# Performance work log

Hardware: AMD Instinct MI355X
Metric: run time of the kernel (lower is better)

Reference implementation:

```python
import jax, jax.numpy as jnp
import numpy as np

B, T, NV, DEG, E = 64, 256, 20000, 8, 128
NSEG, NBUCKET = NV * DEG, 288
F_DIST, F_DIR, F_TT, HID = 50, 50, 50, 100
FEED = 2 * E + F_DIST + F_DIR  # 356


def setup_inputs() -> dict:
    key = jax.random.key(0)
    ks = jax.random.split(key, 32)
    s = 1.0 / np.sqrt(E)
    return {
        "xs_padded": jax.random.randint(ks[0], (B, T), 0, NV),
        "lengths": jax.random.randint(ks[1], (B,), 8, T + 1),
        "xs_actions": jax.random.randint(ks[2], (B, T - 1), 0, DEG),
        "destinations": jax.random.randint(ks[3], (B,), 0, NV),
        "adj_list": jax.random.randint(ks[4], (NV, DEG), 0, NV),
        "seg_ids": jax.random.randint(ks[5], (NV, DEG), 0, NSEG),
        "start_time": 42,
        "locations": jax.random.normal(ks[6], (NV, 2)),
        "time_dist_seg": jax.random.uniform(ks[7], (NSEG, NBUCKET)) * 10.0,
        "emb": jax.random.normal(ks[8], (NV + 2, E)) * 0.01,
        "Wq": jax.random.normal(ks[9], (E, E)) * s,
        "Wk": jax.random.normal(ks[10], (E, E)) * s,
        "Wv": jax.random.normal(ks[11], (E, E)) * s,
        "Wo": jax.random.normal(ks[12], (E, E)) * s,
        "dist_W": jax.random.normal(ks[13], (1, F_DIST)),
        "dist_b": jnp.zeros((F_DIST,)),
        "dir_W": jax.random.normal(ks[14], (2, F_DIR)) * 0.7,
        "dir_b": jnp.zeros((F_DIR,)),
        "tt_W": jax.random.normal(ks[15], (1, F_TT)),
        "tt_b": jnp.zeros((F_TT,)),
        "ob_W1": jax.random.normal(ks[16], (F_TT, F_TT // 2)) * (1.0 / np.sqrt(F_TT)),
        "ob_b1": jnp.zeros((F_TT // 2,)),
        "ob_W2": jax.random.normal(ks[17], (F_TT // 2, 1)) * (1.0 / np.sqrt(F_TT // 2)),
        "ob_b2": jnp.zeros((1,)),
        "om_W1": jax.random.normal(ks[18], (FEED, HID)) * (1.0 / np.sqrt(FEED)),
        "om_b1": jnp.zeros((HID,)),
        "om_W2": jax.random.normal(ks[19], (HID, HID // 2)) * (1.0 / np.sqrt(HID)),
        "om_b2": jnp.zeros((HID // 2,)),
        "om_W3": jax.random.normal(ks[20], (HID // 2, 1)) * (1.0 / np.sqrt(HID // 2)),
        "om_b3": jnp.zeros((1,)),
    }


def reference(xs_padded, lengths, xs_actions, destinations, adj_list, seg_ids,
              start_time, locations, time_dist_seg, emb, Wq, Wk, Wv, Wo,
              dist_W, dist_b, dir_W, dir_b, tt_W, tt_b,
              ob_W1, ob_b1, ob_W2, ob_b2,
              om_W1, om_b1, om_W2, om_b2, om_W3, om_b3):
    # --- embeddings + causal/padding-masked self-attention (flash_att) ---
    x_e = emb[xs_padded]                                       # [B,T,E]
    q, k, v = x_e @ Wq, x_e @ Wk, x_e @ Wv
    scores = jnp.einsum('bqe,bke->bqk', q, k) / jnp.sqrt(jnp.float32(E))
    causal = jnp.triu(jnp.ones((T, T), bool), 1)
    pad = jnp.arange(T)[None, :] >= lengths[:, None]           # key padding [B,T]
    scores = jnp.where(causal[None] | pad[:, None, :], -1e9, scores)
    hidden = jnp.einsum('bqk,bke->bqe', jax.nn.softmax(scores, axis=-1), v) @ Wo

    # --- irregular neighbor gather: route_neighbors only filled for t < len-1 ---
    valid_t = jnp.arange(T)[None, :] < (lengths - 1)[:, None]  # [B,T]
    rn = jnp.where(valid_t[:, :, None], adj_list[xs_padded], 0)  # [B,T,DEG]

    # --- distance to destination feature ---
    dest_c = locations[destinations][:, None, None, :]         # [B,1,1,2]
    nbr_c = locations[rn]                                      # [B,T,DEG,2]
    dist = jnp.abs(nbr_c - dest_c).sum(-1, keepdims=True) * 100.0
    dist_f = dist @ dist_W + dist_b

    # --- direction (unit vector) feature ---
    vec = nbr_c - locations[xs_padded][:, :, None, :]
    unit = vec / (jnp.linalg.norm(vec, axis=-1, keepdims=True) + 1e-8)
    dir_f = unit @ dir_W + dir_b

    # --- travel-time lookup + masked whitening ---
    nmask = rn != 0
    tt = time_dist_seg[seg_ids[xs_padded], start_time]         # [B,T,DEG]
    mf = nmask.astype(tt.dtype)
    cnt = mf.sum()
    mean = (tt * mf).sum() / cnt
    var = (((tt - mean) ** 2) * mf).sum() / (cnt - 1.0)        # unbiased, like torch.std
    tt = (tt - mean) / (jnp.sqrt(var) + 1e-6)
    tt_f = (tt[..., None] @ tt_W + tt_b) * mf[..., None]

    # --- fuse and score neighbors ---
    hid_e = jnp.broadcast_to(hidden[:, :, None, :], (B, T, DEG, E))
    dest_e = jnp.broadcast_to(emb[destinations][:, None, None, :], (B, T, DEG, E))
    feed = jnp.concatenate([hid_e, dist_f, dir_f, dest_e], axis=-1)  # [B,T,DEG,356]

    ob = (jax.nn.relu(tt_f @ ob_W1 + ob_b1) @ ob_W2 + ob_b2).squeeze(-1)
    h1 = jax.nn.relu(feed @ om_W1 + om_b1)
    h2 = jax.nn.relu(h1 @ om_W2 + om_b2)
    logits = (h2 @ om_W3 + om_b3).squeeze(-1) + ob             # [B,T,DEG]

    # --- per-route mean cross-entropy over valid transitions, summed over batch ---
    logp = jax.nn.log_softmax(logits[:, :T - 1], axis=-1)
    nll = -jnp.take_along_axis(logp, xs_actions[..., None], axis=-1).squeeze(-1)
    vmask = (jnp.arange(T - 1)[None, :] < (lengths - 1)[:, None]).astype(nll.dtype)
    per = (nll * vmask).sum(1) / (lengths - 1).astype(nll.dtype)
    return per.sum()
```

## Files before the change

### kernel.cpp

```cpp
#include <hip/hip_runtime.h>
#include <math.h>

#define BB 64
#define TT 256
#define DEG 8
#define EE 128
#define NBUCKET 288
#define HID 100
#define H2 50

constexpr size_t OFF_STATS   = 0;
constexpr size_t OFF_CDIST   = 4;
constexpr size_t OFF_CDIRX   = 104;
constexpr size_t OFF_CDIRY   = 204;
constexpr size_t OFF_BASE    = 304;
constexpr size_t OFF_V25     = 404;
constexpr size_t OFF_C25     = 429;
constexpr size_t OFF_OBZ     = 454;
constexpr size_t OFF_DESTPRE = 456;
constexpr size_t OFF_WF      = 6856;
constexpr size_t OFF_TT      = 32456;
constexpr size_t OFF_Q       = 163528;
constexpr size_t OFF_K       = OFF_Q + 16384 * 128;
constexpr size_t OFF_VP      = OFF_K + 16384 * 128;

__global__ void __launch_bounds__(256) k_setup(
    const int* destinations, const float* emb, const float* Wo,
    const float* dist_W, const float* dist_b, const float* dir_W, const float* dir_b,
    const float* tt_W, const float* tt_b, const float* ob_W1, const float* ob_b1,
    const float* ob_W2, const float* ob_b2, const float* om_W1, const float* om_b1,
    float* ws, float* out) {
    __shared__ float sh[EE];
    int blk = blockIdx.x;
    int j = threadIdx.x;
    if (blk == 0) {
        if (j < 4) ws[OFF_STATS + j] = 0.f;
        if (j == 0) out[0] = 0.f;
        if (j < HID) {
            float cd = 0.f, cx = 0.f, cy = 0.f, bs = om_b1[j];
            for (int f = 0; f < 50; f++) {
                float w1d = om_W1[(128 + f) * HID + j];
                float w1r = om_W1[(178 + f) * HID + j];
                cd += dist_W[f] * w1d;
                bs += dist_b[f] * w1d + dir_b[f] * w1r;
                cx += dir_W[f] * w1r;
                cy += dir_W[50 + f] * w1r;
            }
            ws[OFF_CDIST + j] = cd; ws[OFF_CDIRX + j] = cx;
            ws[OFF_CDIRY + j] = cy; ws[OFF_BASE + j] = bs;
        }
        if (j >= 128 && j < 153) {
            int jj = j - 128;
            float v = 0.f, c = ob_b1[jj];
            for (int i = 0; i < 50; i++) {
                v += tt_W[i] * ob_W1[i * 25 + jj];
                c += tt_b[i] * ob_W1[i * 25 + jj];
            }
            ws[OFF_V25 + jj] = v; ws[OFF_C25 + jj] = c;
        }
        if (j == 200) {
            float z = ob_b2[0];
            for (int i = 0; i < 25; i++) z += fmaxf(ob_b1[i], 0.f) * ob_W2[i];
            ws[OFF_OBZ] = z;
        }
    } else if (blk <= 64) {
        int b = blk - 1;
        if (j < EE) sh[j] = emb[(size_t)destinations[b] * EE + j];
        __syncthreads();
        if (j < HID) {
            float acc = 0.f;
            for (int i = 0; i < EE; i++) acc += sh[i] * om_W1[(228 + i) * HID + j];
            ws[OFF_DESTPRE + b * HID + j] = acc;
        }
    } else {
        int i = blk - 65;
        if (j < EE) sh[j] = Wo[i * EE + j];
        __syncthreads();
        if (j < HID) {
            float acc = 0.f;
            for (int jj = 0; jj < EE; jj++) acc += sh[jj] * om_W1[jj * HID + j];
            ws[OFF_WF + i * HID + j] = acc;
        }
    }
}

__global__ void __launch_bounds__(256) k_mid(
    const int* xs, const int* lengths, const int* adj, const int* seg,
    const int* stime, const float* tds, const float* emb,
    const float* Wq, const float* Wk, const float* Wv, float* ws) {
    __shared__ float smem[2 * 128 * 36 + 32];
    int blk = blockIdx.x;
    int tid = threadIdx.x;
    if (blk < 512) {
        float (*XT)[36]  = (float(*)[36])smem;
        float (*T1T)[36] = (float(*)[36])(smem + 128 * 36);
        int* vids = (int*)(smem + 2 * 128 * 36);
        int r0 = blk * 32;
        if (tid < 32) vids[tid] = xs[r0 + tid];
        __syncthreads();
        for (int c = 0; c < 16; c++) {
            int idx = c * 256 + tid;
            int r = idx >> 7, i = idx & 127;
            XT[i][r] = emb[(size_t)vids[r] * EE + i];
        }
        __syncthreads();
        int cg = tid & 31, rg = tid >> 5;
        const float* Wmats[2] = {Wq, Wk};
        float* Omats[2] = {ws + OFF_Q, ws + OFF_K};
        for (int mtx = 0; mtx < 2; mtx++) {
            const float* W = Wmats[mtx];
            float acc[4][4];
            #pragma unroll
            for (int a = 0; a < 4; a++)
                #pragma unroll
                for (int bb = 0; bb < 4; bb++) acc[a][bb] = 0.f;
            #pragma unroll 4
            for (int i = 0; i < EE; i++) {
                float4 av = *(const float4*)&XT[i][rg << 2];
                float4 wv = *(const float4*)&W[i * EE + (cg << 2)];
                acc[0][0] += av.x * wv.x; acc[0][1] += av.x * wv.y; acc[0][2] += av.x * wv.z; acc[0][3] += av.x * wv.w;
                acc[1][0] += av.y * wv.x; acc[1][1] += av.y * wv.y; acc[1][2] += av.y * wv.z; acc[1][3] += av.y * wv.w;
                acc[2][0] += av.z * wv.x; acc[2][1] += av.z * wv.y; acc[2][2] += av.z * wv.z; acc[2][3] += av.z * wv.w;
                acc[3][0] += av.w * wv.x; acc[3][1] += av.w * wv.y; acc[3][2] += av.w * wv.z; acc[3][3] += av.w * wv.w;
            }
            float* O = Omats[mtx];
            #pragma unroll
            for (int jj = 0; jj < 4; jj++)
                *(float4*)&O[(size_t)(r0 + (rg << 2) + jj) * EE + (cg << 2)] =
                    make_float4(acc[jj][0], acc[jj][1], acc[jj][2], acc[jj][3]);
        }
        {
            float acc[4][4];
            #pragma unroll
            for (int a = 0; a < 4; a++)
                #pragma unroll
                for (int bb = 0; bb < 4; bb++) acc[a][bb] = 0.f;
            #pragma unroll 4
            for (int i = 0; i < EE; i++) {
                float4 av = *(const float4*)&XT[i][rg << 2];
                float4 wv = *(const float4*)&Wv[i * EE + (cg << 2)];
                acc[0][0] += av.x * wv.x; acc[0][1] += av.x * wv.y; acc[0][2] += av.x * wv.z; acc[0][3] += av.x * wv.w;
                acc[1][0] += av.y * wv.x; acc[1][1] += av.y * wv.y; acc[1][2] += av.y * wv.z; acc[1][3] += av.y * wv.w;
                acc[2][0] += av.z * wv.x; acc[2][1] += av.z * wv.y; acc[2][2] += av.z * wv.z; acc[2][3] += av.z * wv.w;
                acc[3][0] += av.w * wv.x; acc[3][1] += av.w * wv.y; acc[3][2] += av.w * wv.z; acc[3][3] += av.w * wv.w;
            }
            #pragma unroll
            for (int jj = 0; jj < 4; jj++)
                #pragma unroll
                for (int ii = 0; ii < 4; ii++)
                    T1T[(cg << 2) + ii][(rg << 2) + jj] = acc[jj][ii];
        }
        __syncthreads();
        if (cg < 25) {
            const float* WF = ws + OFF_WF;
            float acc[4][4];
            #pragma unroll
            for (int a = 0; a < 4; a++)
                #pragma unroll
                for (int bb = 0; bb < 4; bb++) acc[a][bb] = 0.f;
            #pragma unroll 4
            for (int i = 0; i < EE; i++) {
                float4 av = *(const float4*)&T1T[i][rg << 2];
                float4 wv = *(const float4*)&WF[i * HID + (cg << 2)];
                acc[0][0] += av.x * wv.x; acc[0][1] += av.x * wv.y; acc[0][2] += av.x * wv.z; acc[0][3] += av.x * wv.w;
                acc[1][0] += av.y * wv.x; acc[1][1] += av.y * wv.y; acc[1][2] += av.y * wv.z; acc[1][3] += av.y * wv.w;
                acc[2][0] += av.z * wv.x; acc[2][1] += av.z * wv.y; acc[2][2] += av.z * wv.z; acc[2][3] += av.z * wv.w;
                acc[3][0] += av.w * wv.x; acc[3][1] += av.w * wv.y; acc[3][2] += av.w * wv.z; acc[3][3] += av.w * wv.w;
            }
            float* VP = ws + OFF_VP;
            #pragma unroll
            for (int jj = 0; jj < 4; jj++)
                *(float4*)&VP[(size_t)(r0 + (rg << 2) + jj) * HID + (cg << 2)] =
                    make_float4(acc[jj][0], acc[jj][1], acc[jj][2], acc[jj][3]);
        }
    } else {
        float* rs = smem; float* rq = smem + 256; float* rc = smem + 512;
        int st = *stime;
        float lsum = 0.f, lsq = 0.f, lcnt = 0.f;
        int total = BB * TT * DEG;
        for (int idx = (blk - 512) * 256 + tid; idx < total; idx += 256 * 256) {
            int d = idx & 7;
            int bt = idx >> 3;
            int t = bt & 255;
            int b = bt >> 8;
            int len = lengths[b];
            if (t >= len - 1) continue;
            int v = xs[bt];
            int sg = seg[v * DEG + d];
            float tt = tds[(size_t)sg * NBUCKET + st];
            ws[OFF_TT + idx] = tt;
            int a = adj[v * DEG + d];
            if (a != 0) { lsum += tt; lsq += tt * tt; lcnt += 1.f; }
        }
        rs[tid] = lsum; rq[tid] = lsq; rc[tid] = lcnt;
        __syncthreads();
        for (int s = 128; s > 0; s >>= 1) {
            if (tid < s) { rs[tid] += rs[tid + s]; rq[tid] += rq[tid + s]; rc[tid] += rc[tid + s]; }
            __syncthreads();
        }
        if (tid == 0) {
            atomicAdd(&ws[OFF_STATS + 0], rs[0]);
            atomicAdd(&ws[OFF_STATS + 1], rq[0]);
            atomicAdd(&ws[OFF_STATS + 2], rc[0]);
        }
    }
}

__global__ void __launch_bounds__(256) k_attnfinal(
    const int* lengths, const int* xs, const int* xs_actions,
    const int* destinations, const int* adj, const float* locations,
    const float* om_W2, const float* om_b2, const float* om_W3, const float* om_b3,
    const float* ob_W2, const float* ob_b2,
    float* ws, float* out) {
    int blk = blockIdx.x;
    int tile = 31 - (blk >> 6);
    int b = blk & 63;
    int t0 = tile << 3;
    int len = lengths[b];
    if (t0 >= len - 1) return;
    int nqv = len - 1 - t0; if (nqv > 8) nqv = 8;
    int nk = t0 + 8;
    __shared__ float smem[13160];
    float (*H1P)[104] = (float(*)[104])smem;
    float (*Qs)[132]  = (float(*)[132])(smem + 832);
    float (*S)[260]   = (float(*)[260])(smem + 1888);
    float (*Vs)[104]  = (float(*)[104])(smem + 3968);
    float (*pacc)[8]  = (float(*)[8])(smem + 10624);
    float (*W2s)[56]  = (float(*)[56])(smem + 832);
    float (*h1T)[64]  = (float(*)[64])(smem + 6432);
    float* distR = smem + 12832;
    float* uxR   = smem + 12896;
    float* uyR   = smem + 12960;
    float* obR   = smem + 13024;
    float* lgS   = smem + 13088;
    float* nllS  = smem + 13152;
    int tid = threadIdx.x;
    if (tid < 8) nllS[tid] = 0.f;
    {
        const float* Qg = ws + OFF_Q + (size_t)(b * TT + t0) * EE;
        int r = tid >> 5, c4 = (tid & 31) << 2;
        *(float4*)&Qs[r][c4] = *(const float4*)&Qg[r * EE + c4];
    }
    __syncthreads();
    {
        const float* Kg = ws + OFF_K + (size_t)(b * TT) * EE;
        int w = tid >> 6;
        int key = (tid >> 2) & 15, chunk = tid & 3;
        int coff = chunk << 5;
        for (int k0 = w << 4; k0 < nk; k0 += 64) {
            int kk = k0 + key;
            if (kk < nk) {
                float4 kf[8];
                const float4* Kr = (const float4*)&Kg[(size_t)kk * EE + coff];
                #pragma unroll
                for (int j = 0; j < 8; j++) kf[j] = Kr[j];
                #pragma unroll
                for (int q = 0; q < 8; q++) {
                    const float4* qr = (const float4*)&Qs[q][coff];
                    float s = 0.f;
                    #pragma unroll
                    for (int j = 0; j < 8; j++) {
                        float4 a = qr[j], x = kf[j];
                        s += a.x * x.x + a.y * x.y + a.z * x.z + a.w * x.w;
                    }
                    s += __shfl_xor(s, 1, 64);
                    s += __shfl_xor(s, 2, 64);
                    if (chunk == 0) S[q][kk] = s * 0.08838834764831845f;
                }
            }
        }
    }
    __syncthreads();
    if (tid < 128) {
        int q = tid >> 4, li = tid & 15;
        int tq = t0 + q;
        float sreg[16];
        float mx = -1e30f;
        #pragma unroll
        for (int m = 0; m < 16; m++) {
            int k = li + (m << 4);
            float sv = (k < nk && k <= tq) ? S[q][k] : -1e30f;
            sreg[m] = sv;
            mx = fmaxf(mx, sv);
        }
        #pragma unroll
        for (int o = 1; o < 16; o <<= 1) mx = fmaxf(mx, __shfl_xor(mx, o, 16));
        float ls = 0.f;
        #pragma unroll
        for (int m = 0; m < 16; m++) {
            float p = __expf(sreg[m] - mx);
            sreg[m] = p; ls += p;
        }
        #pragma unroll
        for (int o = 1; o < 16; o <<= 1) ls += __shfl_xor(ls, o, 16);
        float inv = 1.f / ls;
        #pragma unroll
        for (int m = 0; m < 16; m++) S[q][li + (m << 4)] = sreg[m] * inv;
    }
    __syncthreads();
    {
        int kc = tid >> 7;
        int q = (tid >> 4) & 7, cg = tid & 15;
        float acc[8];
        #pragma unroll
        for (int j = 0; j < 8; j++) acc[j] = 0.f;
        const float* VPg = ws + OFF_VP + (size_t)(b * TT) * HID;
        for (int vt0 = 0; vt0 < nk; vt0 += 64) {
            __syncthreads();
            int nrow = nk - vt0; if (nrow > 64) nrow = 64;
            for (int idx = tid; idx < nrow * 25; idx += 256) {
                int r = idx / 25, c4 = (idx - r * 25) << 2;
                *(float4*)&Vs[r][c4] = *(const float4*)&VPg[(size_t)(vt0 + r) * HID + c4];
            }
            __syncthreads();
            int base = vt0 + (kc << 5);
            int kmax = nk - base; if (kmax > 32) kmax = 32;
            if (cg < 13) {
                for (int k = 0; k < kmax; k++) {
                    float p = S[q][base + k];
                    const float4* vr = (const float4*)&Vs[(kc << 5) + k][cg << 3];
                    float4 v0 = vr[0], v1 = vr[1];
                    acc[0] += p * v0.x; acc[1] += p * v0.y;
                    acc[2] += p * v0.z; acc[3] += p * v0.w;
                    acc[4] += p * v1.x; acc[5] += p * v1.y;
                    acc[6] += p * v1.z; acc[7] += p * v1.w;
                }
            }
        }
        if (kc == 1 && cg < 13) {
            float* pp = pacc[(q << 4) + cg];
            #pragma unroll
            for (int j = 0; j < 8; j++) pp[j] = acc[j];
        }
        __syncthreads();
        if (kc == 0 && cg < 13) {
            const float* pp = pacc[(q << 4) + cg];
            const float* BASEv = ws + OFF_BASE;
            const float* DP = ws + OFF_DESTPRE + b * HID;
            int c0 = cg << 3;
            #pragma unroll
            for (int j = 0; j < 8; j++) {
                int c = c0 + j;
                if (c < HID) H1P[q][c] = acc[j] + pp[j] + BASEv[c] + DP[c];
            }
        }
    }
    __syncthreads();
    for (int idx = tid; idx < 5600; idx += 256) {
        int mm = idx / 56, n = idx - mm * 56;
        W2s[mm][n] = (n < H2) ? om_W2[mm * H2 + n] : 0.f;
    }
    float smean, sdinv;
    {
        float sum = ws[OFF_STATS], sq = ws[OFF_STATS + 1], cnt = ws[OFF_STATS + 2];
        smean = sum / cnt;
        float var = (sq - cnt * smean * smean) / (cnt - 1.f);
        sdinv = 1.f / (sqrtf(var) + 1e-6f);
    }
    if (tid < 64) {
        int ql = tid >> 3, d = tid & 7;
        int t = t0 + ql;
        int bt = b * TT + t;
        int v = xs[bt];
        int a = adj[v * DEG + d];
        float nbx = locations[2 * a], nby = locations[2 * a + 1];
        int dst = destinations[b];
        float dxl = locations[2 * dst], dyl = locations[2 * dst + 1];
        float cxl = locations[2 * v], cyl = locations[2 * v + 1];
        distR[tid] = (fabsf(nbx - dxl) + fabsf(nby - dyl)) * 100.f;
        float vx = nbx - cxl, vy = nby - cyl;
        float nrm = sqrtf(vx * vx + vy * vy) + 1e-8f;
        uxR[tid] = vx / nrm; uyR[tid] = vy / nrm;
        float ttn = (ws[OFF_TT + (size_t)bt * 8 + d] - smean) * sdinv;
        float obp = 0.f;
        for (int j = 0; j < 25; j++)
            obp += fmaxf(ttn * ws[OFF_V25 + j] + ws[OFF_C25 + j], 0.f) * ob_W2[j];
        obR[tid] = (a != 0) ? (obp + ob_b2[0]) : ws[OFF_OBZ];
    }
    __syncthreads();
    {
        int r = tid & 63, mq = tid >> 6;
        int qa = r >> 3;
        float dv = distR[r], ux = uxR[r], uy = uyR[r];
        const float* CD = ws + OFF_CDIST;
        const float* CX = ws + OFF_CDIRX;
        const float* CY = ws + OFF_CDIRY;
        const float* Hq = H1P[qa];
        int m0 = mq * 25;
        #pragma unroll 5
        for (int mi = 0; mi < 25; mi++) {
            int m = m0 + mi;
            float pre = Hq[m] + dv * CD[m] + ux * CX[m] + uy * CY[m];
            h1T[m][r] = fmaxf(pre, 0.f);
        }
    }
    __syncthreads();
    {
        int lane = tid & 63, w = tid >> 6;
        int rg = (w << 2) | (lane >> 4);
        int half = (lane >> 3) & 1;
        int cg = lane & 7;
        int r0 = rg << 2, n0 = cg << 3;
        float facc[4][8];
        #pragma unroll
        for (int jr = 0; jr < 4; jr++)
            #pragma unroll
            for (int k = 0; k < 8; k++) facc[jr][k] = 0.f;
        if (cg < 7) {
            int m0 = half * 50;
            #pragma unroll 5
            for (int mi = 0; mi < 50; mi++) {
                int m = m0 + mi;
                float4 hv = *(const float4*)&h1T[m][r0];
                float4 w0 = *(const float4*)&W2s[m][n0];
                float4 w1 = *(const float4*)&W2s[m][n0 + 4];
                facc[0][0] += hv.x * w0.x; facc[0][1] += hv.x * w0.y; facc[0][2] += hv.x * w0.z; facc[0][3] += hv.x * w0.w;
                facc[0][4] += hv.x * w1.x; facc[0][5] += hv.x * w1.y; facc[0][6] += hv.x * w1.z; facc[0][7] += hv.x * w1.w;
                facc[1][0] += hv.y * w0.x; facc[1][1] += hv.y * w0.y; facc[1][2] += hv.y * w0.z; facc[1][3] += hv.y * w0.w;
                facc[1][4] += hv.y * w1.x; facc[1][5] += hv.y * w1.y; facc[1][6] += hv.y * w1.z; facc[1][7] += hv.y * w1.w;
                facc[2][0] += hv.z * w0.x; facc[2][1] += hv.z * w0.y; facc[2][2] += hv.z * w0.z; facc[2][3] += hv.z * w0.w;
                facc[2][4] += hv.z * w1.x; facc[2][5] += hv.z * w1.y; facc[2][6] += hv.z * w1.z; facc[2][7] += hv.z * w1.w;
                facc[3][0] += hv.w * w0.x; facc[3][1] += hv.w * w0.y; facc[3][2] += hv.w * w0.z; facc[3][3] += hv.w * w0.w;
                facc[3][4] += hv.w * w1.x; facc[3][5] += hv.w * w1.y; facc[3][6] += hv.w * w1.z; facc[3][7] += hv.w * w1.w;
            }
        }
        #pragma unroll
        for (int jr = 0; jr < 4; jr++)
            #pragma unroll
            for (int k = 0; k < 8; k++)
                facc[jr][k] += __shfl_xor(facc[jr][k], 8, 64);
        float parts[4] = {0.f, 0.f, 0.f, 0.f};
        if (cg < 7) {
            float b2v[8], w3v[8];
            #pragma unroll
            for (int k = 0; k < 8; k++) {
                int n = n0 + k;
                b2v[k] = (n < H2) ? om_b2[n] : 0.f;
                w3v[k] = (n < H2) ? om_W3[n] : 0.f;
            }
            #pragma unroll
            for (int jr = 0; jr < 4; jr++) {
                float part = 0.f;
                #pragma unroll
                for (int k = 0; k < 8; k++)
                    part += fmaxf(facc[jr][k] + b2v[k], 0.f) * w3v[k];
                parts[jr] = part;
            }
        }
        float ob3 = om_b3[0];
        #pragma unroll
        for (int jr = 0; jr < 4; jr++) {
            float part = parts[jr];
            part += __shfl_xor(part, 1, 64);
            part += __shfl_xor(part, 2, 64);
            part += __shfl_xor(part, 4, 64);
            if ((lane & 15) == 0) lgS[r0 + jr] = part + ob3 + obR[r0 + jr];
        }
    }
    __syncthreads();
    if (tid < 8) {
        int qa = tid;
        if (qa < nqv) {
            float lg[8];
            float mxl = -1e30f;
            #pragma unroll
            for (int d = 0; d < 8; d++) {
                lg[d] = lgS[(qa << 3) + d];
                mxl = fmaxf(mxl, lg[d]);
            }
            int act = xs_actions[b * (TT - 1) + t0 + qa];
            float se = 0.f, sel = 0.f;
            #pragma unroll
            for (int d = 0; d < 8; d++) {
                se += __expf(lg[d] - mxl);
                if (d == act) sel = lg[d];
            }
            float nll = mxl + __logf(se) - sel;
            nllS[qa] = nll / (float)(len - 1);
        }
    }
    __syncthreads();
    if (tid == 0) {
        float s = 0.f;
        #pragma unroll
        for (int i = 0; i < 8; i++) s += nllS[i];
        atomicAdd(out, s);
    }
}

extern "C" void kernel_launch(void* const* d_in, const int* in_sizes, int n_in,
                              void* d_out, int out_size, void* d_ws, size_t ws_size,
                              hipStream_t stream) {
    const int* xs_padded    = (const int*)d_in[0];
    const int* lengths      = (const int*)d_in[1];
    const int* xs_actions   = (const int*)d_in[2];
    const int* destinations = (const int*)d_in[3];
    const int* adj_list     = (const int*)d_in[4];
    const int* seg_ids      = (const int*)d_in[5];
    const int* start_time   = (const int*)d_in[6];
    const float* locations  = (const float*)d_in[7];
    const float* tds        = (const float*)d_in[8];
    const float* emb        = (const float*)d_in[9];
    const float* Wq         = (const float*)d_in[10];
    const float* Wk         = (const float*)d_in[11];
    const float* Wv         = (const float*)d_in[12];
    const float* Wo         = (const float*)d_in[13];
    const float* dist_W     = (const float*)d_in[14];
    const float* dist_b     = (const float*)d_in[15];
    const float* dir_W      = (const float*)d_in[16];
    const float* dir_b      = (const float*)d_in[17];
    const float* tt_W       = (const float*)d_in[18];
    const float* tt_b       = (const float*)d_in[19];
    const float* ob_W1      = (const float*)d_in[20];
    const float* ob_b1      = (const float*)d_in[21];
    const float* ob_W2      = (const float*)d_in[22];
    const float* ob_b2      = (const float*)d_in[23];
    const float* om_W1      = (const float*)d_in[24];
    const float* om_b1      = (const float*)d_in[25];
    const float* om_W2      = (const float*)d_in[26];
    const float* om_b2      = (const float*)d_in[27];
    const float* om_W3      = (const float*)d_in[28];
    const float* om_b3      = (const float*)d_in[29];
    float* ws  = (float*)d_ws;
    float* out = (float*)d_out;

    k_setup<<<193, 256, 0, stream>>>(destinations, emb, Wo, dist_W, dist_b,
                                     dir_W, dir_b, tt_W, tt_b, ob_W1, ob_b1,
                                     ob_W2, ob_b2, om_W1, om_b1, ws, out);
    k_mid<<<768, 256, 0, stream>>>(xs_padded, lengths, adj_list, seg_ids,
                                   start_time, tds, emb, Wq, Wk, Wv, ws);
    k_attnfinal<<<BB * 32, 256, 0, stream>>>(
        lengths, xs_padded, xs_actions, destinations, adj_list, locations,
        om_W2, om_b2, om_W3, om_b3, ob_W2, ob_b2, ws, out);
}
```

Baseline: 442.5 us.

## Shrink attention-final shared memory to raise occupancy and stream weights from global

Cuts the k_attnfinal shared footprint from about 52KB to about 21KB. It drops the V staging tile, the padded W2 copy and the h1T buffer. P·V now reads value rows straight from global memory, and om_W2 is pre-padded to 56 columns once in k_setup and read from global/cache inside the MLP loop. The first-layer ReLU activations are recomputed inline from H1P plus per-neighbor coefficients instead of being stored. The feature computation moves onto otherwise idle threads during softmax, and launch bounds ask for 6 blocks per CU. The trade is more global/L2 traffic and recomputation in exchange for higher occupancy and fewer barriers.

```diff
diff --git a/kernel.cpp b/kernel.cpp
--- a/kernel.cpp
+++ b/kernel.cpp
@@ -19,6 +19,7 @@
 constexpr size_t OFF_OBZ     = 454;
 constexpr size_t OFF_DESTPRE = 456;
 constexpr size_t OFF_WF      = 6856;
+constexpr size_t OFF_W2P     = 19656;
 constexpr size_t OFF_TT      = 32456;
 constexpr size_t OFF_Q       = 163528;
 constexpr size_t OFF_K       = OFF_Q + 16384 * 128;
@@ -29,7 +30,7 @@
     const float* dist_W, const float* dist_b, const float* dir_W, const float* dir_b,
     const float* tt_W, const float* tt_b, const float* ob_W1, const float* ob_b1,
     const float* ob_W2, const float* ob_b2, const float* om_W1, const float* om_b1,
-    float* ws, float* out) {
+    const float* om_W2, float* ws, float* out) {
     __shared__ float sh[EE];
     int blk = blockIdx.x;
     int j = threadIdx.x;
@@ -72,7 +73,7 @@
             for (int i = 0; i < EE; i++) acc += sh[i] * om_W1[(228 + i) * HID + j];
             ws[OFF_DESTPRE + b * HID + j] = acc;
         }
-    } else {
+    } else if (blk <= 192) {
         int i = blk - 65;
         if (j < EE) sh[j] = Wo[i * EE + j];
         __syncthreads();
@@ -80,6 +81,11 @@
             float acc = 0.f;
             for (int jj = 0; jj < EE; jj++) acc += sh[jj] * om_W1[jj * HID + j];
             ws[OFF_WF + i * HID + j] = acc;
+        }
+    } else {
+        for (int idx = j; idx < 5600; idx += 256) {
+            int m = idx / 56, n = idx - m * 56;
+            ws[OFF_W2P + idx] = (n < H2) ? om_W2[m * H2 + n] : 0.f;
         }
     }
 }
@@ -206,10 +212,10 @@
     }
 }
 
-__global__ void __launch_bounds__(256) k_attnfinal(
+__global__ void __launch_bounds__(256, 6) k_attnfinal(
     const int* lengths, const int* xs, const int* xs_actions,
     const int* destinations, const int* adj, const float* locations,
-    const float* om_W2, const float* om_b2, const float* om_W3, const float* om_b3,
+    const float* om_b2, const float* om_W3, const float* om_b3,
     const float* ob_W2, const float* ob_b2,
     float* ws, float* out) {
     int blk = blockIdx.x;
@@ -220,20 +226,18 @@
     if (t0 >= len - 1) return;
     int nqv = len - 1 - t0; if (nqv > 8) nqv = 8;
     int nk = t0 + 8;
-    __shared__ float smem[13160];
-    float (*H1P)[104] = (float(*)[104])smem;
-    float (*Qs)[132]  = (float(*)[132])(smem + 832);
-    float (*S)[260]   = (float(*)[260])(smem + 1888);
-    float (*Vs)[104]  = (float(*)[104])(smem + 3968);
-    float (*pacc)[8]  = (float(*)[8])(smem + 10624);
-    float (*W2s)[56]  = (float(*)[56])(smem + 832);
-    float (*h1T)[64]  = (float(*)[64])(smem + 6432);
-    float* distR = smem + 12832;
-    float* uxR   = smem + 12896;
-    float* uyR   = smem + 12960;
-    float* obR   = smem + 13024;
-    float* lgS   = smem + 13088;
-    float* nllS  = smem + 13152;
+    __shared__ float smem[5264];
+    float (*H1P)[100] = (float(*)[100])smem;
+    float (*Qs)[132]  = (float(*)[132])(smem + 800);
+    float (*S)[260]   = (float(*)[260])(smem + 1856);
+    float (*pacc)[8]  = (float(*)[8])(smem + 3936);
+    float* CFs   = smem + 800;
+    float* distR = smem + 4936;
+    float* uxR   = smem + 5000;
+    float* uyR   = smem + 5064;
+    float* obR   = smem + 5128;
+    float* lgS   = smem + 5192;
+    float* nllS  = smem + 5256;
     int tid = threadIdx.x;
     if (tid < 8) nllS[tid] = 0.f;
     {
@@ -296,69 +300,21 @@
         float inv = 1.f / ls;
         #pragma unroll
         for (int m = 0; m < 16; m++) S[q][li + (m << 4)] = sreg[m] * inv;
-    }
-    __syncthreads();
-    {
-        int kc = tid >> 7;
-        int q = (tid >> 4) & 7, cg = tid & 15;
-        float acc[8];
-        #pragma unroll
-        for (int j = 0; j < 8; j++) acc[j] = 0.f;
-        const float* VPg = ws + OFF_VP + (size_t)(b * TT) * HID;
-        for (int vt0 = 0; vt0 < nk; vt0 += 64) {
-            __syncthreads();
-            int nrow = nk - vt0; if (nrow > 64) nrow = 64;
-            for (int idx = tid; idx < nrow * 25; idx += 256) {
-                int r = idx / 25, c4 = (idx - r * 25) << 2;
-                *(float4*)&Vs[r][c4] = *(const float4*)&VPg[(size_t)(vt0 + r) * HID + c4];
-            }
-            __syncthreads();
-            int base = vt0 + (kc << 5);
-            int kmax = nk - base; if (kmax > 32) kmax = 32;
-            if (cg < 13) {
-                for (int k = 0; k < kmax; k++) {
-                    float p = S[q][base + k];
-                    const float4* vr = (const float4*)&Vs[(kc << 5) + k][cg << 3];
-                    float4 v0 = vr[0], v1 = vr[1];
-                    acc[0] += p * v0.x; acc[1] += p * v0.y;
-                    acc[2] += p * v0.z; acc[3] += p * v0.w;
-                    acc[4] += p * v1.x; acc[5] += p * v1.y;
-                    acc[6] += p * v1.z; acc[7] += p * v1.w;
-                }
-            }
-        }
-        if (kc == 1 && cg < 13) {
-            float* pp = pacc[(q << 4) + cg];
-            #pragma unroll
-            for (int j = 0; j < 8; j++) pp[j] = acc[j];
-        }
-        __syncthreads();
-        if (kc == 0 && cg < 13) {
-            const float* pp = pacc[(q << 4) + cg];
-            const float* BASEv = ws + OFF_BASE;
-            const float* DP = ws + OFF_DESTPRE + b * HID;
-            int c0 = cg << 3;
-            #pragma unroll
-            for (int j = 0; j < 8; j++) {
-                int c = c0 + j;
-                if (c < HID) H1P[q][c] = acc[j] + pp[j] + BASEv[c] + DP[c];
-            }
-        }
-    }
-    __syncthreads();
-    for (int idx = tid; idx < 5600; idx += 256) {
-        int mm = idx / 56, n = idx - mm * 56;
-        W2s[mm][n] = (n < H2) ? om_W2[mm * H2 + n] : 0.f;
-    }
-    float smean, sdinv;
-    {
-        float sum = ws[OFF_STATS], sq = ws[OFF_STATS + 1], cnt = ws[OFF_STATS + 2];
-        smean = sum / cnt;
-        float var = (sq - cnt * smean * smean) / (cnt - 1.f);
-        sdinv = 1.f / (sqrtf(var) + 1e-6f);
-    }
-    if (tid < 64) {
-        int ql = tid >> 3, d = tid & 7;
+    } else if (tid < 192) {
+        const float* CD = ws + OFF_CDIST;
+        const float* CX = ws + OFF_CDIRX;
+        const float* CY = ws + OFF_CDIRY;
+        for (int idx = tid - 128; idx < 400; idx += 64) {
+            int m = idx >> 2, c = idx & 3;
+            float v = 0.f;
+            if (c == 0) v = CD[m];
+            else if (c == 1) v = CX[m];
+            else if (c == 2) v = CY[m];
+            CFs[idx] = v;
+        }
+    } else {
+        int fid = tid - 192;
+        int ql = fid >> 3, d = fid & 7;
         int t = t0 + ql;
         int bt = b * TT + t;
         int v = xs[bt];
@@ -367,31 +323,59 @@
         int dst = destinations[b];
         float dxl = locations[2 * dst], dyl = locations[2 * dst + 1];
         float cxl = locations[2 * v], cyl = locations[2 * v + 1];
-        distR[tid] = (fabsf(nbx - dxl) + fabsf(nby - dyl)) * 100.f;
+        distR[fid] = (fabsf(nbx - dxl) + fabsf(nby - dyl)) * 100.f;
         float vx = nbx - cxl, vy = nby - cyl;
         float nrm = sqrtf(vx * vx + vy * vy) + 1e-8f;
-        uxR[tid] = vx / nrm; uyR[tid] = vy / nrm;
+        uxR[fid] = vx / nrm; uyR[fid] = vy / nrm;
+        float sum = ws[OFF_STATS], sq = ws[OFF_STATS + 1], cnt = ws[OFF_STATS + 2];
+        float smean = sum / cnt;
+        float var = (sq - cnt * smean * smean) / (cnt - 1.f);
+        float sdinv = 1.f / (sqrtf(var) + 1e-6f);
         float ttn = (ws[OFF_TT + (size_t)bt * 8 + d] - smean) * sdinv;
         float obp = 0.f;
         for (int j = 0; j < 25; j++)
             obp += fmaxf(ttn * ws[OFF_V25 + j] + ws[OFF_C25 + j], 0.f) * ob_W2[j];
-        obR[tid] = (a != 0) ? (obp + ob_b2[0]) : ws[OFF_OBZ];
+        obR[fid] = (a != 0) ? (obp + ob_b2[0]) : ws[OFF_OBZ];
     }
     __syncthreads();
     {
-        int r = tid & 63, mq = tid >> 6;
-        int qa = r >> 3;
-        float dv = distR[r], ux = uxR[r], uy = uyR[r];
-        const float* CD = ws + OFF_CDIST;
-        const float* CX = ws + OFF_CDIRX;
-        const float* CY = ws + OFF_CDIRY;
-        const float* Hq = H1P[qa];
-        int m0 = mq * 25;
-        #pragma unroll 5
-        for (int mi = 0; mi < 25; mi++) {
-            int m = m0 + mi;
-            float pre = Hq[m] + dv * CD[m] + ux * CX[m] + uy * CY[m];
-            h1T[m][r] = fmaxf(pre, 0.f);
+        int kc = tid >> 7;
+        int q = (tid >> 4) & 7, cg = tid & 15;
+        float acc[8];
+        #pragma unroll
+        for (int j = 0; j < 8; j++) acc[j] = 0.f;
+        if (cg < 13) {
+            const float* VPg = ws + OFF_VP + (size_t)(b * TT) * HID;
+            int o0 = cg << 3;
+            int o1 = o0 + 4; if (o1 > 96) o1 = 96;
+            #pragma unroll 2
+            for (int k = kc; k < nk; k += 2) {
+                float p = S[q][k];
+                const float* vr = &VPg[(size_t)k * HID];
+                float4 v0 = *(const float4*)&vr[o0];
+                float4 v1 = *(const float4*)&vr[o1];
+                acc[0] += p * v0.x; acc[1] += p * v0.y;
+                acc[2] += p * v0.z; acc[3] += p * v0.w;
+                acc[4] += p * v1.x; acc[5] += p * v1.y;
+                acc[6] += p * v1.z; acc[7] += p * v1.w;
+            }
+        }
+        if (kc == 1 && cg < 13) {
+            float* pp = &pacc[(q << 4) + cg][0];
+            *(float4*)&pp[0] = make_float4(acc[0], acc[1], acc[2], acc[3]);
+            *(float4*)&pp[4] = make_float4(acc[4], acc[5], acc[6], acc[7]);
+        }
+        __syncthreads();
+        if (kc == 0 && cg < 13) {
+            const float* pp = &pacc[(q << 4) + cg][0];
+            const float* BASEv = ws + OFF_BASE;
+            const float* DP = ws + OFF_DESTPRE + b * HID;
+            int c0 = cg << 3;
+            #pragma unroll
+            for (int j = 0; j < 8; j++) {
+                int c = c0 + j;
+                if (c < HID) H1P[q][c] = acc[j] + pp[j] + BASEv[c] + DP[c];
+            }
         }
     }
     __syncthreads();
@@ -401,27 +385,38 @@
         int half = (lane >> 3) & 1;
         int cg = lane & 7;
         int r0 = rg << 2, n0 = cg << 3;
+        const float* Hq = &smem[(rg >> 1) * 100];
+        float4 dv4 = *(const float4*)&distR[r0];
+        float4 ux4 = *(const float4*)&uxR[r0];
+        float4 uy4 = *(const float4*)&uyR[r0];
         float facc[4][8];
         #pragma unroll
         for (int jr = 0; jr < 4; jr++)
             #pragma unroll
             for (int k = 0; k < 8; k++) facc[jr][k] = 0.f;
         if (cg < 7) {
+            const float* W2P = ws + OFF_W2P;
             int m0 = half * 50;
-            #pragma unroll 5
+            #pragma unroll 2
             for (int mi = 0; mi < 50; mi++) {
                 int m = m0 + mi;
-                float4 hv = *(const float4*)&h1T[m][r0];
-                float4 w0 = *(const float4*)&W2s[m][n0];
-                float4 w1 = *(const float4*)&W2s[m][n0 + 4];
-                facc[0][0] += hv.x * w0.x; facc[0][1] += hv.x * w0.y; facc[0][2] += hv.x * w0.z; facc[0][3] += hv.x * w0.w;
-                facc[0][4] += hv.x * w1.x; facc[0][5] += hv.x * w1.y; facc[0][6] += hv.x * w1.z; facc[0][7] += hv.x * w1.w;
-                facc[1][0] += hv.y * w0.x; facc[1][1] += hv.y * w0.y; facc[1][2] += hv.y * w0.z; facc[1][3] += hv.y * w0.w;
-                facc[1][4] += hv.y * w1.x; facc[1][5] += hv.y * w1.y; facc[1][6] += hv.y * w1.z; facc[1][7] += hv.y * w1.w;
-                facc[2][0] += hv.z * w0.x; facc[2][1] += hv.z * w0.y; facc[2][2] += hv.z * w0.z; facc[2][3] += hv.z * w0.w;
-                facc[2][4] += hv.z * w1.x; facc[2][5] += hv.z * w1.y; facc[2][6] += hv.z * w1.z; facc[2][7] += hv.z * w1.w;
-                facc[3][0] += hv.w * w0.x; facc[3][1] += hv.w * w0.y; facc[3][2] += hv.w * w0.z; facc[3][3] += hv.w * w0.w;
-                facc[3][4] += hv.w * w1.x; facc[3][5] += hv.w * w1.y; facc[3][6] += hv.w * w1.z; facc[3][7] += hv.w * w1.w;
+                float4 cf = *(const float4*)&CFs[m << 2];
+                float hq = Hq[m];
+                float h0 = fmaxf(hq + dv4.x * cf.x + ux4.x * cf.y + uy4.x * cf.z, 0.f);
+                float h1 = fmaxf(hq + dv4.y * cf.x + ux4.y * cf.y + uy4.y * cf.z, 0.f);
+                float h2 = fmaxf(hq + dv4.z * cf.x + ux4.z * cf.y + uy4.z * cf.z, 0.f);
+                float h3 = fmaxf(hq + dv4.w * cf.x + ux4.w * cf.y + uy4.w * cf.z, 0.f);
+                const float* wrow = &W2P[m * 56 + n0];
+                float4 w0 = *(const float4*)&wrow[0];
+                float4 w1 = *(const float4*)&wrow[4];
+                facc[0][0] += h0 * w0.x; facc[0][1] += h0 * w0.y; facc[0][2] += h0 * w0.z; facc[0][3] += h0 * w0.w;
+                facc[0][4] += h0 * w1.x; facc[0][5] += h0 * w1.y; facc[0][6] += h0 * w1.z; facc[0][7] += h0 * w1.w;
+                facc[1][0] += h1 * w0.x; facc[1][1] += h1 * w0.y; facc[1][2] += h1 * w0.z; facc[1][3] += h1 * w0.w;
+                facc[1][4] += h1 * w1.x; facc[1][5] += h1 * w1.y; facc[1][6] += h1 * w1.z; facc[1][7] += h1 * w1.w;
+                facc[2][0] += h2 * w0.x; facc[2][1] += h2 * w0.y; facc[2][2] += h2 * w0.z; facc[2][3] += h2 * w0.w;
+                facc[2][4] += h2 * w1.x; facc[2][5] += h2 * w1.y; facc[2][6] += h2 * w1.z; facc[2][7] += h2 * w1.w;
+                facc[3][0] += h3 * w0.x; facc[3][1] += h3 * w0.y; facc[3][2] += h3 * w0.z; facc[3][3] += h3 * w0.w;
+                facc[3][4] += h3 * w1.x; facc[3][5] += h3 * w1.y; facc[3][6] += h3 * w1.z; facc[3][7] += h3 * w1.w;
             }
         }
         #pragma unroll
@@ -524,12 +519,12 @@
     float* ws  = (float*)d_ws;
     float* out = (float*)d_out;
 
-    k_setup<<<193, 256, 0, stream>>>(destinations, emb, Wo, dist_W, dist_b,
+    k_setup<<<194, 256, 0, stream>>>(destinations, emb, Wo, dist_W, dist_b,
                                      dir_W, dir_b, tt_W, tt_b, ob_W1, ob_b1,
-                                     ob_W2, ob_b2, om_W1, om_b1, ws, out);
+                                     ob_W2, ob_b2, om_W1, om_b1, om_W2, ws, out);
     k_mid<<<768, 256, 0, stream>>>(xs_padded, lengths, adj_list, seg_ids,
                                    start_time, tds, emb, Wq, Wk, Wv, ws);
     k_attnfinal<<<BB * 32, 256, 0, stream>>>(
         lengths, xs_padded, xs_actions, destinations, adj_list, locations,
-        om_W2, om_b2, om_W3, om_b3, ob_W2, ob_b2, ws, out);
+        om_b2, om_W3, om_b3, ob_W2, ob_b2, ws, out);
 }
```

Result: slower. 459.3 us (+3.8%).
